# Performance work log

Hardware: AMD Instinct MI355X
Metric: run time of the kernel (lower is better)

Reference implementation:

```python
import jax, jax.numpy as jnp
import numpy as np
from jax import lax

B, T, D, H, C, FF, NH = 256, 48, 89, 128, 64, 64, 8
HD = C // NH


def _pos_encoding(n, c):
    pos = jnp.arange(n, dtype=jnp.float32)[:, None]
    div = jnp.exp(jnp.arange(0, c, 2, dtype=jnp.float32) * (-np.log(10000.0) / c))
    pe = jnp.zeros((n, c), dtype=jnp.float32)
    pe = pe.at[:, 0::2].set(jnp.sin(pos * div))
    pe = pe.at[:, 1::2].set(jnp.cos(pos * div))
    return pe


def _ln(x, g, b):
    m = x.mean(-1, keepdims=True)
    v = ((x - m) ** 2).mean(-1, keepdims=True)
    return (x - m) / jnp.sqrt(v + 1e-5) * g + b


def setup_inputs():
    key = jax.random.key(0)
    ks = iter(jax.random.split(key, 64))
    def n(shape, s=0.05):
        return (jax.random.normal(next(ks), shape) * s).astype(jnp.float32)
    x = jax.random.normal(next(ks), (B, T, D), dtype=jnp.float32)
    mask = (jax.random.uniform(next(ks), (B, T, D)) < 0.8).astype(jnp.float32)
    deltas = (jax.random.uniform(next(ks), (B, T, D)) * 5.0).astype(jnp.float32)
    last_obs = jax.random.normal(next(ks), (B, T, D), dtype=jnp.float32)
    medians = (jax.random.uniform(next(ks), (D,)) * 2.0).astype(jnp.float32)
    return dict(
        x=x, mask=mask, deltas=deltas, last_obs=last_obs, medians=medians,
        W_dh=n((H, D)), b_dh=n((H,)), W_dx=n((D, D)), b_dx=n((D,)),
        W_hist=n((D, H)), b_hist=n((D,)), W_feat=n((D, D)), b_feat=n((D,)),
        W_wc=n((D, 2 * D)), b_wc=n((D,)), W_wo=n((D, D)), b_wo=n((D,)),
        W_cls=n((1, H)), b_cls=n((1,)),
        W_ih=n((3 * H, 2 * D)), W_hh=n((3 * H, H)), b_ih=n((3 * H,)), b_hh=n((3 * H,)),
        W_inp=n((C, D)), b_inp=n((C,)), W_op1=n((H, C)), b_op1=n((H,)),
        W_op2=n((2 * T,)), b_op2=n((1,)),
        attn_in_w=n((3 * C, C)), attn_in_b=n((3 * C,)),
        attn_out_w=n((C, C)), attn_out_b=n((C,)),
        ln1_g=jnp.ones((C,)), ln1_b=jnp.zeros((C,)),
        ln2_g=jnp.ones((C,)), ln2_b=jnp.zeros((C,)),
        ff1_w=n((FF, C)), ff1_b=n((FF,)), ff2_w=n((C, FF)), ff2_b=n((C,)))


def _forward(x, mask, deltas, last_obs, medians,
             W_dh, b_dh, W_dx, b_dx, W_hist, b_hist, W_feat, b_feat,
             W_wc, b_wc, W_wo, b_wo, W_cls, b_cls,
             W_ih, W_hh, b_ih, b_hh, W_inp, b_inp, W_op1, b_op1, W_op2, b_op2,
             attn_in_w, attn_in_b, attn_out_w, attn_out_b,
             ln1_g, ln1_b, ln2_g, ln2_b, ff1_w, ff1_b, ff2_w, ff2_b):
    # Decay_obs: weight = 0.5*(1 - tanh(sign(dd)*|linear(dd)|))
    dd = deltas - medians[None, None, :]
    wd = dd @ W_wo.T + b_wo
    decay_factor = 0.5 * (1.0 - jnp.tanh(jnp.sign(dd) * jnp.abs(wd)))

    # time encoder: 1x1 conv projection + positional encoding
    pe = _pos_encoding(T, C)[None]                      # [1,T,C]
    d_lo = last_obs @ W_inp.T + b_inp + pe              # [B,T,C]
    d_df = decay_factor @ W_inp.T + b_inp + pe          # [B,T,C]
    data = jnp.concatenate([d_lo, d_df], axis=1)        # [B,2T,C]

    # torch TransformerEncoderLayer (post-norm, gelu, dropout off).
    # NOTE: layer is NOT batch_first, so attention runs over axis 0 (B);
    # axis 1 (2T) behaves as the batch — faithful to the source.
    qkv = data @ attn_in_w.T + attn_in_b                # [B,2T,3C]
    q, k, v = jnp.split(qkv, 3, axis=-1)
    q = q.reshape(B, 2 * T, NH, HD)
    k = k.reshape(B, 2 * T, NH, HD)
    v = v.reshape(B, 2 * T, NH, HD)
    scores = jnp.einsum('snhd,tnhd->nhst', q, k) / np.sqrt(HD)
    probs = jax.nn.softmax(scores, axis=-1)
    o = jnp.einsum('nhst,tnhd->snhd', probs, v).reshape(B, 2 * T, C)
    o = o @ attn_out_w.T + attn_out_b
    x1 = _ln(data + o, ln1_g, ln1_b)
    ff = jax.nn.gelu(x1 @ ff1_w.T + ff1_b, approximate=False) @ ff2_w.T + ff2_b
    data = _ln(x1 + ff, ln2_g, ln2_b)                   # [B,2T,C]

    data = data @ W_op1.T + b_op1                       # [B,2T,H]
    h0 = jnp.einsum('bnh,n->bh', data, W_op2) + b_op2[0]  # Conv1d(2T->1,k=1)

    diag_w = jnp.diagonal(W_dx)                         # temp_decay_x diag mask
    offdiag = 1.0 - jnp.eye(D, dtype=x.dtype)

    def step(carry, inp):
        h, loss = carry
        x_t, m_t, d_t = inp
        gamma_h = jnp.exp(-jax.nn.relu(d_t @ W_dh.T + b_dh))
        h = h * gamma_h
        x_h = h @ W_hist.T + b_hist
        x_r = m_t * x_t + (1.0 - m_t) * x_h
        xu = x_r @ (W_feat * offdiag).T + b_feat
        gamma_x = jnp.exp(-jax.nn.relu(d_t * diag_w + b_dx))
        beta = jnp.concatenate([gamma_x, m_t], axis=-1) @ W_wc.T + b_wc
        x_comb = beta * xu + (1.0 - beta) * x_h
        loss = loss + jnp.sum(jnp.abs(x_t - x_comb) * m_t) / (jnp.sum(m_t) + 1e-5)
        x_imp_t = m_t * x_t + (1.0 - m_t) * x_comb
        gi = jnp.concatenate([x_imp_t, m_t], axis=-1) @ W_ih.T + b_ih
        gh = h @ W_hh.T + b_hh
        ir, iz, ig = jnp.split(gi, 3, axis=-1)
        hr, hz, hg = jnp.split(gh, 3, axis=-1)
        r = jax.nn.sigmoid(ir + hr)
        z = jax.nn.sigmoid(iz + hz)
        g = jnp.tanh(ig + r * hg)
        h = (1.0 - z) * g + z * h
        return (h, loss), (x_imp_t, h)

    xs = (x.transpose(1, 0, 2), mask.transpose(1, 0, 2), deltas.transpose(1, 0, 2))
    (h, x_loss), (x_imp_T, hid_T) = lax.scan(step, (h0, jnp.zeros((), x.dtype)), xs)
    x_imp = x_imp_T.transpose(1, 0, 2)                  # [B,T,D]
    hiddens = hid_T.transpose(1, 0, 2)                  # [B,T,H]

    y_out = h @ W_cls.T + b_cls
    y_score = jax.nn.sigmoid(y_out)
    return x_imp, x_loss, hiddens, y_out, y_score


def reference(x, mask, deltas, last_obs, medians,
              W_dh, b_dh, W_dx, b_dx, W_hist, b_hist, W_feat, b_feat,
              W_wc, b_wc, W_wo, b_wo, W_cls, b_cls,
              W_ih, W_hh, b_ih, b_hh, W_inp, b_inp, W_op1, b_op1, W_op2, b_op2,
              attn_in_w, attn_in_b, attn_out_w, attn_out_b,
              ln1_g, ln1_b, ln2_g, ln2_b, ff1_w, ff1_b, ff2_w, ff2_b):
    return _forward(x, mask, deltas, last_obs, medians,
                    W_dh, b_dh, W_dx, b_dx, W_hist, b_hist, W_feat, b_feat,
                    W_wc, b_wc, W_wo, b_wo, W_cls, b_cls,
                    W_ih, W_hh, b_ih, b_hh, W_inp, b_inp, W_op1, b_op1, W_op2, b_op2,
                    attn_in_w, attn_in_b, attn_out_w, attn_out_b,
                    ln1_g, ln1_b, ln2_g, ln2_b, ff1_w, ff1_b, ff2_w, ff2_b)
```

## Files before the change

kernel.cpp:

```cpp
#include <hip/hip_runtime.h>
#include <math.h>

#define B_  256
#define T_  48
#define D_  89
#define H_  128
#define C_  64
#define NH_ 8
#define HD_ 8
#define N2T 96

#define XIMP_OFF 0
#define LOSS_OFF 1093632
#define HID_OFF  1093633
#define Y_OFF    2666497
#define YS_OFF   2666753

typedef unsigned int uint_t;
typedef _Float16 h2_t __attribute__((ext_vector_type(2)));

__device__ __forceinline__ float wave_sum64(float v) {
    v += __shfl_xor(v, 32);
    v += __shfl_xor(v, 16);
    v += __shfl_xor(v, 8);
    v += __shfl_xor(v, 4);
    v += __shfl_xor(v, 2);
    v += __shfl_xor(v, 1);
    return v;
}

__device__ __forceinline__ uint_t packh2(float lo, float hi) {
    union { h2_t h; uint_t u; } c;
    c.h.x = (_Float16)lo;
    c.h.y = (_Float16)hi;
    return c.u;
}
__device__ __forceinline__ h2_t as_h2(uint_t u) {
    union { uint_t u; h2_t h; } c;
    c.u = u;
    return c.h;
}
__device__ __forceinline__ float dot2h(uint_t w, uint_t a, float acc) {
#if __has_builtin(__builtin_amdgcn_fdot2)
    return __builtin_amdgcn_fdot2(as_h2(w), as_h2(a), acc, false);
#else
    h2_t hw = as_h2(w), ha = as_h2(a);
    return fmaf((float)hw.y, (float)ha.y, fmaf((float)hw.x, (float)ha.x, acc));
#endif
}
__device__ __forceinline__ float sigm(float v) { return 1.f / (1.f + __expf(-v)); }

#define DOT96H(W, A, acc) do { \
    _Pragma("unroll") \
    for (int it_ = 0; it_ < 3; ++it_) { \
        int idx_ = jj + 8 * it_; \
        uint2 w_ = ((const uint2*)(W))[idx_]; \
        uint2 a_ = ((const uint2*)(A))[idx_]; \
        acc = dot2h(w_.x, a_.x, acc); \
        acc = dot2h(w_.y, a_.y, acc); \
    } } while (0)

#define DOT128H(W, A, acc) do { \
    _Pragma("unroll") \
    for (int it_ = 0; it_ < 4; ++it_) { \
        int idx_ = jj + 8 * it_; \
        uint2 w_ = ((const uint2*)(W))[idx_]; \
        uint2 a_ = ((const uint2*)(A))[idx_]; \
        acc = dot2h(w_.x, a_.x, acc); \
        acc = dot2h(w_.y, a_.y, acc); \
    } } while (0)

__device__ __forceinline__ void tr_f32(const float* __restrict__ s, float* __restrict__ d,
                                       int li, int R, int C) {
    int r = li / C, c = li - r * C;
    d[c * R + r] = s[li];
}

__global__ void k_wprep(const float* W_wo, const float* W_inp, const float* ain_w,
                        const float* aout_w, const float* ff1_w, const float* ff2_w,
                        const float* W_op1,
                        float* W_woT, float* W_inpT, float* ain_T,
                        float* aout_T, float* ff1_T, float* ff2_T, float* op1_T,
                        const float* __restrict__ W_dh, const float* __restrict__ W_hist,
                        const float* __restrict__ W_ih, const float* __restrict__ W_hh,
                        uint_t* __restrict__ wdh_h, uint_t* __restrict__ whist_h,
                        uint_t* __restrict__ wihx_h, uint_t* __restrict__ wihm_h,
                        uint_t* __restrict__ whh_h) {
    int i = blockIdx.x * 256 + threadIdx.x;
    if (i < 7921)         tr_f32(W_wo,   W_woT,  i,          89, 89);
    else if (i < 13617)   tr_f32(W_inp,  W_inpT, i - 7921,   64, 89);
    else if (i < 25905)   tr_f32(ain_w,  ain_T,  i - 13617, 192, 64);
    else if (i < 30001)   tr_f32(aout_w, aout_T, i - 25905,  64, 64);
    else if (i < 34097)   tr_f32(ff1_w,  ff1_T,  i - 30001,  64, 64);
    else if (i < 38193)   tr_f32(ff2_w,  ff2_T,  i - 34097,  64, 64);
    else if (i < 46385)   tr_f32(W_op1,  op1_T,  i - 38193, 128, 64);
    else {
        int p = i - 46385;
        if (p < 6144) {
            int r = p / 48, c = p - r * 48;
            const float* src = W_dh + r * 89;
            float lo = (c < 45) ? src[2 * c] : 0.f;
            float hi = (c < 44) ? src[2 * c + 1] : 0.f;
            wdh_h[p] = packh2(lo, hi);
        } else if (p < 11840) {
            int j = p - 6144;
            int r = j / 64, c = j - r * 64;
            const float* src = W_hist + r * 128;
            whist_h[j] = packh2(src[2 * c], src[2 * c + 1]);
        } else if (p < 30272) {
            int j = p - 11840;
            int r = j / 48, c = j - r * 48;
            const float* src = W_ih + (size_t)r * 178;
            float lo = (c < 45) ? src[2 * c] : 0.f;
            float hi = (c < 44) ? src[2 * c + 1] : 0.f;
            wihx_h[j] = packh2(lo, hi);
        } else if (p < 48704) {
            int j = p - 30272;
            int r = j / 48, c = j - r * 48;
            const float* src = W_ih + (size_t)r * 178 + 89;
            float lo = (c < 45) ? src[2 * c] : 0.f;
            float hi = (c < 44) ? src[2 * c + 1] : 0.f;
            wihm_h[j] = packh2(lo, hi);
        } else if (p < 73280) {
            int j = p - 48704;
            int r = j / 64, c = j - r * 64;
            const float* src = W_hh + (size_t)r * 128;
            whh_h[j] = packh2(src[2 * c], src[2 * c + 1]);
        }
    }
}

__global__ void k_phaseA(const float* __restrict__ last_obs,
                         const float* __restrict__ deltas,
                         const float* __restrict__ medians,
                         const float* __restrict__ W_woT, const float* __restrict__ b_wo,
                         const float* __restrict__ W_inpT, const float* __restrict__ b_inp,
                         const float* __restrict__ ain_T, const float* __restrict__ ain_b,
                         float* __restrict__ data,
                         float* __restrict__ qb, float* __restrict__ kb, float* __restrict__ vb) {
    int bt = blockIdx.x;
    int b = bt / T_;
    int t = bt - b * T_;
    __shared__ float dd[D_], lo[D_], dec[D_];
    __shared__ float rows[2][C_];
    int tid = threadIdx.x;
    int base = (b * T_ + t) * D_;
    if (tid < D_) {
        float dv = deltas[base + tid] - medians[tid];
        dd[tid] = dv;
        lo[tid] = last_obs[base + tid];
    }
    __syncthreads();
    if (tid < D_) {
        float a0 = b_wo[tid], a1 = 0.f;
        for (int j = 0; j < 88; j += 2) {
            a0 = fmaf(dd[j],     W_woT[j * D_ + tid],       a0);
            a1 = fmaf(dd[j + 1], W_woT[(j + 1) * D_ + tid], a1);
        }
        float acc = fmaf(dd[88], W_woT[88 * D_ + tid], a0) + a1;
        float dv = dd[tid];
        float s = (dv > 0.f) ? 1.f : ((dv < 0.f) ? -1.f : 0.f);
        dec[tid] = 0.5f * (1.f - tanhf(s * fabsf(acc)));
    }
    __syncthreads();
    int c = tid & 63;
    int half = tid >> 6;
    {
        const float* src = half ? dec : lo;
        float a0 = b_inp[c], a1 = 0.f;
        for (int j = 0; j < 88; j += 2) {
            a0 = fmaf(src[j],     W_inpT[j * C_ + c],       a0);
            a1 = fmaf(src[j + 1], W_inpT[(j + 1) * C_ + c], a1);
        }
        float acc = fmaf(src[88], W_inpT[88 * C_ + c], a0) + a1;
        int i = c >> 1;
        float div = __expf((float)i * -0.28782313662425574f);
        float ang = (float)t * div;
        float pe = (c & 1) ? cosf(ang) : sinf(ang);
        float val = acc + pe;
        rows[half][c] = val;
        data[((b * N2T) + half * T_ + t) * C_ + c] = val;
    }
    __syncthreads();
    #pragma unroll
    for (int it = 0; it < 3; ++it) {
        int idx = it * 128 + tid;
        int h2 = idx / 192;
        int col = idx - h2 * 192;
        const float* row = rows[h2];
        float a0 = ain_b[col], a1 = 0.f;
        #pragma unroll
        for (int j = 0; j < 64; j += 2) {
            a0 = fmaf(row[j],     ain_T[j * 192 + col],       a0);
            a1 = fmaf(row[j + 1], ain_T[(j + 1) * 192 + col], a1);
        }
        float acc = a0 + a1;
        int n = h2 * T_ + t;
        int part = col >> 6;
        int cc = col & 63;
        int hh = cc >> 3, d = cc & 7;
        float* dst = (part == 0) ? qb : ((part == 1) ? kb : vb);
        dst[(((n * NH_ + hh) * B_ + b) * HD_) + d] = acc;
    }
}

__global__ void k_attn(const float* __restrict__ qb, const float* __restrict__ kb,
                       const float* __restrict__ vb, float* __restrict__ attnO) {
    int n = blockIdx.x >> 3;
    int h = blockIdx.x & 7;
    __shared__ float k_lds[B_][HD_ + 1];
    __shared__ float v_lds[B_][HD_ + 1];
    int s = threadIdx.x;
    const float scale = 0.35355339059327373f;
    size_t base = ((size_t)blockIdx.x * B_ + s) * HD_;
    float q[HD_];
    #pragma unroll
    for (int d = 0; d < HD_; ++d) q[d] = qb[base + d] * scale;
    #pragma unroll
    for (int d = 0; d < HD_; ++d) { k_lds[s][d] = kb[base + d]; v_lds[s][d] = vb[base + d]; }
    __syncthreads();
    float m = -1e30f;
    #pragma unroll 4
    for (int t = 0; t < B_; ++t) {
        float sc = 0.f;
        #pragma unroll
        for (int d = 0; d < HD_; ++d) sc = fmaf(q[d], k_lds[t][d], sc);
        m = fmaxf(m, sc);
    }
    float l = 0.f;
    float acc[HD_] = {0.f, 0.f, 0.f, 0.f, 0.f, 0.f, 0.f, 0.f};
    #pragma unroll 2
    for (int t = 0; t < B_; ++t) {
        float sc = 0.f;
        #pragma unroll
        for (int d = 0; d < HD_; ++d) sc = fmaf(q[d], k_lds[t][d], sc);
        float p = __expf(sc - m);
        l += p;
        #pragma unroll
        for (int d = 0; d < HD_; ++d) acc[d] = fmaf(p, v_lds[t][d], acc[d]);
    }
    float inv = 1.f / l;
    float* op = attnO + ((size_t)s * N2T + n) * C_ + h * HD_;
    #pragma unroll
    for (int d = 0; d < HD_; ++d) op[d] = acc[d] * inv;
}

__global__ void k_transform(const float* __restrict__ data,
                            const float* __restrict__ attnO,
                            const float* __restrict__ aout_T, const float* __restrict__ aout_b,
                            const float* __restrict__ ln1_g, const float* __restrict__ ln1_b,
                            const float* __restrict__ ff1_T, const float* __restrict__ ff1_b,
                            const float* __restrict__ ff2_T, const float* __restrict__ ff2_b,
                            const float* __restrict__ ln2_g, const float* __restrict__ ln2_b,
                            const float* __restrict__ op1_T, const float* __restrict__ b_op1,
                            float* __restrict__ val) {
    int bn = blockIdx.x;
    __shared__ float orow[C_], x1s[C_], hbuf[C_], x2s[C_];
    int c = threadIdx.x;
    float d0 = data[bn * C_ + c];
    orow[c] = attnO[bn * C_ + c];
    __syncthreads();
    float a0 = aout_b[c], a1 = 0.f;
    #pragma unroll
    for (int j = 0; j < C_; j += 2) {
        a0 = fmaf(orow[j],     aout_T[j * C_ + c],       a0);
        a1 = fmaf(orow[j + 1], aout_T[(j + 1) * C_ + c], a1);
    }
    float r = d0 + a0 + a1;
    float mean = wave_sum64(r) * (1.f / 64.f);
    float df = r - mean;
    float var = wave_sum64(df * df) * (1.f / 64.f);
    float x1 = df * rsqrtf(var + 1e-5f) * ln1_g[c] + ln1_b[c];
    x1s[c] = x1;
    __syncthreads();
    a0 = ff1_b[c]; a1 = 0.f;
    #pragma unroll
    for (int j = 0; j < C_; j += 2) {
        a0 = fmaf(x1s[j],     ff1_T[j * C_ + c],       a0);
        a1 = fmaf(x1s[j + 1], ff1_T[(j + 1) * C_ + c], a1);
    }
    float accf = a0 + a1;
    float ge = 0.5f * accf * (1.f + erff(accf * 0.7071067811865475f));
    hbuf[c] = ge;
    __syncthreads();
    a0 = ff2_b[c]; a1 = 0.f;
    #pragma unroll
    for (int j = 0; j < C_; j += 2) {
        a0 = fmaf(hbuf[j],     ff2_T[j * C_ + c],       a0);
        a1 = fmaf(hbuf[j + 1], ff2_T[(j + 1) * C_ + c], a1);
    }
    float r2 = x1 + a0 + a1;
    float mean2 = wave_sum64(r2) * (1.f / 64.f);
    float df2 = r2 - mean2;
    float var2 = wave_sum64(df2 * df2) * (1.f / 64.f);
    float x2 = df2 * rsqrtf(var2 + 1e-5f) * ln2_g[c] + ln2_b[c];
    x2s[c] = x2;
    __syncthreads();
    #pragma unroll
    for (int rep = 0; rep < 2; ++rep) {
        int k = c + rep * 64;
        float b0 = b_op1[k], b1 = 0.f;
        #pragma unroll
        for (int j = 0; j < C_; j += 2) {
            b0 = fmaf(x2s[j],     op1_T[j * H_ + k],       b0);
            b1 = fmaf(x2s[j + 1], op1_T[(j + 1) * H_ + k], b1);
        }
        val[(size_t)bn * H_ + k] = b0 + b1;
    }
}

__global__ void k_reduce_h0(const float* __restrict__ val,
                            const float* __restrict__ W_op2, const float* __restrict__ b_op2,
                            float* __restrict__ h0) {
    int b = blockIdx.x;
    int h = threadIdx.x;
    float a0 = b_op2[0], a1 = 0.f;
    for (int n = 0; n < N2T; n += 2) {
        a0 = fmaf(val[((size_t)b * N2T + n) * H_ + h],       W_op2[n],     a0);
        a1 = fmaf(val[((size_t)b * N2T + n + 1) * H_ + h],   W_op2[n + 1], a1);
    }
    h0[b * H_ + h] = a0 + a1;
}

__global__ void k_den(const float* __restrict__ mask, float* __restrict__ den) {
    int t = blockIdx.x;
    int tid = threadIdx.x;
    float s = 0.f;
    const int total = B_ * D_;
    for (int i = tid; i < total; i += 256) {
        int b = i / D_;
        int d = i - b * D_;
        s += mask[(b * T_ + t) * D_ + d];
    }
    s = wave_sum64(s);
    __shared__ float red[4];
    if ((tid & 63) == 0) red[tid >> 6] = s;
    __syncthreads();
    if (tid == 0) den[t] = red[0] + red[1] + red[2] + red[3];
}

__global__ __launch_bounds__(1024)
void k_scan(const float* __restrict__ x, const float* __restrict__ mask,
            const float* __restrict__ deltas,
            const uint_t* __restrict__ wdh_h, const float* __restrict__ b_dh,
            const float* __restrict__ W_dx, const float* __restrict__ b_dx,
            const uint_t* __restrict__ whist_h, const float* __restrict__ b_hist,
            const float* __restrict__ W_feat, const float* __restrict__ b_feat,
            const float* __restrict__ W_wc, const float* __restrict__ b_wc,
            const uint_t* __restrict__ wihx_h, const uint_t* __restrict__ wihm_h,
            const uint_t* __restrict__ whh_h,
            const float* __restrict__ b_ih, const float* __restrict__ b_hh,
            const float* __restrict__ W_cls, const float* __restrict__ b_cls,
            const float* __restrict__ h0,
            float* __restrict__ out, float* __restrict__ num_part) {
    int b = blockIdx.x;
    int tid = threadIdx.x;
    int wave = tid >> 6;
    int lane = tid & 63;
    int oo = lane >> 3;
    int jj = lane & 7;

    __shared__ __align__(16) float h_s[H_];
    __shared__ __align__(16) uint_t h_h[64];
    __shared__ __align__(16) float xt_s[96], m_s[96], xh_s[96], beta_s[96], diff_s[96];
    __shared__ __align__(16) uint_t dt_h[48], gx_h[48], m_h[48], xr_h[48], ximp_h[48];
    __shared__ __align__(16) float gis[384], ghs[384];
    __shared__ __align__(16) uint_t wwcg_l[89 * 48];
    __shared__ __align__(16) uint_t wwcm_l[89 * 48];
    __shared__ __align__(16) uint_t wfeat_l[89 * 48];

    float dxw = 0.f, dxb = 0.f;
    if (tid >= 384 && tid < 473) {
        int o = tid - 384;
        dxw = W_dx[o * 90];
        dxb = b_dx[o];
    }

    for (int i = tid; i < 89 * 48; i += 1024) {
        int r = i / 48, c = i - r * 48;
        const float* wr = W_wc + (size_t)r * 178;
        float lo = (c < 45) ? wr[2 * c] : 0.f;
        float hi = (c < 44) ? wr[2 * c + 1] : 0.f;
        wwcg_l[i] = packh2(lo, hi);
        const float* wm = wr + 89;
        float lo2 = (c < 45) ? wm[2 * c] : 0.f;
        float hi2 = (c < 44) ? wm[2 * c + 1] : 0.f;
        wwcm_l[i] = packh2(lo2, hi2);
        const float* wf = W_feat + r * 89;
        float lo3 = (c < 45 && 2 * c != r) ? wf[2 * c] : 0.f;
        float hi3 = (c < 44 && 2 * c + 1 != r) ? wf[2 * c + 1] : 0.f;
        wfeat_l[i] = packh2(lo3, hi3);
    }
    if (tid < 128) {
        float hv = h0[b * H_ + tid];
        h_s[tid] = hv;
        float nx = __shfl_down(hv, 1);
        if ((tid & 1) == 0) h_h[tid >> 1] = packh2(hv, nx);
    }
    if (tid == 500) {
        #pragma unroll
        for (int k = 45; k < 48; ++k) {
            dt_h[k] = 0u; gx_h[k] = 0u; m_h[k] = 0u; xr_h[k] = 0u; ximp_h[k] = 0u;
        }
    }
    {
        int nb = b * T_ * D_;
        if (tid >= 128 && tid < 217) xt_s[tid - 128] = x[nb + tid - 128];
        else if (tid >= 256 && tid < 345) {
            int o = tid - 256;
            float mv = mask[nb + o];
            m_s[o] = mv;
            float nx = __shfl_down(mv, 1);
            if (o + 1 >= 89) nx = 0.f;
            if ((o & 1) == 0) m_h[o >> 1] = packh2(mv, nx);
        } else if (tid >= 384 && tid < 473) {
            int o = tid - 384;
            float dv = deltas[nb + o];
            float gxv = __expf(-fmaxf(dv * dxw + dxb, 0.f));
            float nd = __shfl_down(dv, 1);
            float ng = __shfl_down(gxv, 1);
            if (o + 1 >= 89) { nd = 0.f; ng = 0.f; }
            if ((o & 1) == 0) { dt_h[o >> 1] = packh2(dv, nd); gx_h[o >> 1] = packh2(gxv, ng); }
        }
    }
    __syncthreads();

    for (int t = 0; t < T_; ++t) {
        for (int c = wave; c < 76; c += 16) {
            if (c < 16) {
                int o = c * 8 + oo;
                float acc = 0.f;
                DOT96H(wdh_h + o * 48, dt_h, acc);
                acc += __shfl_xor(acc, 1); acc += __shfl_xor(acc, 2); acc += __shfl_xor(acc, 4);
                if (jj == 0) {
                    float hv = h_s[o] * __expf(-fmaxf(acc + b_dh[o], 0.f));
                    h_s[o] = hv;
                    float nx = __shfl_down(hv, 8);
                    if ((oo & 1) == 0) h_h[o >> 1] = packh2(hv, nx);
                }
            } else if (c < 28) {
                int o = (c - 16) * 8 + oo;
                int ro = (o < 89) ? o : 88;
                float acc = 0.f;
                DOT96H(wwcg_l + ro * 48, gx_h, acc);
                DOT96H(wwcm_l + ro * 48, m_h, acc);
                acc += __shfl_xor(acc, 1); acc += __shfl_xor(acc, 2); acc += __shfl_xor(acc, 4);
                if (jj == 0 && o < 89) beta_s[o] = acc + b_wc[o];
            } else {
                int o = (c - 28) * 8 + oo;
                float acc = 0.f;
                DOT96H(wihm_h + o * 48, m_h, acc);
                acc += __shfl_xor(acc, 1); acc += __shfl_xor(acc, 2); acc += __shfl_xor(acc, 4);
                if (jj == 0) gis[o] = acc + b_ih[o];
            }
        }
        __syncthreads();
        for (int c = wave; c < 60; c += 16) {
            if (c < 12) {
                int o = c * 8 + oo;
                int ro = (o < 89) ? o : 88;
                float acc = 0.f;
                DOT128H(whist_h + ro * 64, h_h, acc);
                acc += __shfl_xor(acc, 1); acc += __shfl_xor(acc, 2); acc += __shfl_xor(acc, 4);
                if (jj == 0) {
                    float xh = acc + b_hist[ro];
                    float m = m_s[ro];
                    float xrv = m * xt_s[ro] + (1.f - m) * xh;
                    float nx = __shfl_down(xrv, 8);
                    if (o + 1 >= 89) nx = 0.f;
                    if (o < 89) xh_s[o] = xh;
                    if ((oo & 1) == 0 && o < 89) xr_h[o >> 1] = packh2(xrv, nx);
                }
            } else {
                int o = (c - 12) * 8 + oo;
                float acc = 0.f;
                DOT128H(whh_h + o * 64, h_h, acc);
                acc += __shfl_xor(acc, 1); acc += __shfl_xor(acc, 2); acc += __shfl_xor(acc, 4);
                if (jj == 0) ghs[o] = acc + b_hh[o];
            }
        }
        __syncthreads();
        for (int c = wave; c < 12; c += 16) {
            int o = c * 8 + oo;
            int ro = (o < 89) ? o : 88;
            float xu = 0.f;
            DOT96H(wfeat_l + ro * 48, xr_h, xu);
            xu += __shfl_xor(xu, 1); xu += __shfl_xor(xu, 2); xu += __shfl_xor(xu, 4);
            if (jj == 0) {
                float xuf = xu + b_feat[ro];
                float btf = beta_s[ro];
                float xc = btf * xuf + (1.f - btf) * xh_s[ro];
                float m = m_s[ro];
                float xtv = xt_s[ro];
                float xi = m * xtv + (1.f - m) * xc;
                float nx = __shfl_down(xi, 8);
                if (o + 1 >= 89) nx = 0.f;
                if (o < 89) {
                    out[XIMP_OFF + (b * T_ + t) * D_ + o] = xi;
                    diff_s[o] = fabsf(xtv - xc) * m;
                }
                if ((oo & 1) == 0 && o < 89) ximp_h[o >> 1] = packh2(xi, nx);
            }
        }
        __syncthreads();
        for (int c = wave; c < 48; c += 16) {
            int o = c * 8 + oo;
            float acc = 0.f;
            DOT96H(wihx_h + o * 48, ximp_h, acc);
            acc += __shfl_xor(acc, 1); acc += __shfl_xor(acc, 2); acc += __shfl_xor(acc, 4);
            if (jj == 0) gis[o] += acc;
        }
        __syncthreads();
        if (tid < 128) {
            float r = sigm(gis[tid] + ghs[tid]);
            float z = sigm(gis[128 + tid] + ghs[128 + tid]);
            float g = tanhf(gis[256 + tid] + r * ghs[256 + tid]);
            float hn = (1.f - z) * g + z * h_s[tid];
            h_s[tid] = hn;
            out[HID_OFF + (size_t)(b * T_ + t) * H_ + tid] = hn;
            float nx = __shfl_down(hn, 1);
            if ((tid & 1) == 0) h_h[tid >> 1] = packh2(hn, nx);
        } else if (tid >= 960) {
            int l = tid - 960;
            float s = diff_s[l] + ((l < 25) ? diff_s[64 + l] : 0.f);
            s = wave_sum64(s);
            if (l == 0) num_part[t * B_ + b] = s;
        } else if (t + 1 < T_) {
            int nb = (b * T_ + t + 1) * D_;
            if (tid < 217) xt_s[tid - 128] = x[nb + tid - 128];
            else if (tid >= 256 && tid < 345) {
                int o = tid - 256;
                float mv = mask[nb + o];
                m_s[o] = mv;
                float nx = __shfl_down(mv, 1);
                if (o + 1 >= 89) nx = 0.f;
                if ((o & 1) == 0) m_h[o >> 1] = packh2(mv, nx);
            } else if (tid >= 384 && tid < 473) {
                int o = tid - 384;
                float dv = deltas[nb + o];
                float gxv = __expf(-fmaxf(dv * dxw + dxb, 0.f));
                float nd = __shfl_down(dv, 1);
                float ng = __shfl_down(gxv, 1);
                if (o + 1 >= 89) { nd = 0.f; ng = 0.f; }
                if ((o & 1) == 0) { dt_h[o >> 1] = packh2(dv, nd); gx_h[o >> 1] = packh2(gxv, ng); }
            }
        }
        __syncthreads();
    }
    if (tid < 64) {
        float p = h_s[tid] * W_cls[tid] + h_s[tid + 64] * W_cls[tid + 64];
        p = wave_sum64(p);
        if (tid == 0) {
            float y = p + b_cls[0];
            out[Y_OFF + b] = y;
            out[YS_OFF + b] = 1.f / (1.f + __expf(-y));
        }
    }
}

__global__ void k_loss(const float* __restrict__ num_part, const float* __restrict__ den,
                       float* __restrict__ out) {
    int tid = threadIdx.x;
    float v = 0.f;
    if (tid < T_) {
        float s = 0.f;
        const float* np_ = num_part + tid * B_;
        for (int b = 0; b < B_; ++b) s += np_[b];
        v = s / (den[tid] + 1e-5f);
    }
    v = wave_sum64(v);
    if (tid == 0) out[LOSS_OFF] = v;
}

extern "C" void kernel_launch(void* const* d_in, const int* in_sizes, int n_in,
                              void* d_out, int out_size, void* d_ws, size_t ws_size,
                              hipStream_t stream) {
    const float* x        = (const float*)d_in[0];
    const float* mask     = (const float*)d_in[1];
    const float* deltas   = (const float*)d_in[2];
    const float* last_obs = (const float*)d_in[3];
    const float* medians  = (const float*)d_in[4];
    const float* W_dh  = (const float*)d_in[5];
    const float* b_dh  = (const float*)d_in[6];
    const float* W_dx  = (const float*)d_in[7];
    const float* b_dx  = (const float*)d_in[8];
    const float* W_hist= (const float*)d_in[9];
    const float* b_hist= (const float*)d_in[10];
    const float* W_feat= (const float*)d_in[11];
    const float* b_feat= (const float*)d_in[12];
    const float* W_wc  = (const float*)d_in[13];
    const float* b_wc  = (const float*)d_in[14];
    const float* W_wo  = (const float*)d_in[15];
    const float* b_wo  = (const float*)d_in[16];
    const float* W_cls = (const float*)d_in[17];
    const float* b_cls = (const float*)d_in[18];
    const float* W_ih  = (const float*)d_in[19];
    const float* W_hh  = (const float*)d_in[20];
    const float* b_ih  = (const float*)d_in[21];
    const float* b_hh  = (const float*)d_in[22];
    const float* W_inp = (const float*)d_in[23];
    const float* b_inp = (const float*)d_in[24];
    const float* W_op1 = (const float*)d_in[25];
    const float* b_op1 = (const float*)d_in[26];
    const float* W_op2 = (const float*)d_in[27];
    const float* b_op2 = (const float*)d_in[28];
    const float* attn_in_w  = (const float*)d_in[29];
    const float* attn_in_b  = (const float*)d_in[30];
    const float* attn_out_w = (const float*)d_in[31];
    const float* attn_out_b = (const float*)d_in[32];
    const float* ln1_g = (const float*)d_in[33];
    const float* ln1_b = (const float*)d_in[34];
    const float* ln2_g = (const float*)d_in[35];
    const float* ln2_b = (const float*)d_in[36];
    const float* ff1_w = (const float*)d_in[37];
    const float* ff1_b = (const float*)d_in[38];
    const float* ff2_w = (const float*)d_in[39];
    const float* ff2_b = (const float*)d_in[40];

    float* out = (float*)d_out;
    float* ws = (float*)d_ws;

    float* data  = ws;
    float* qb    = data  + (size_t)B_ * N2T * C_;
    float* kb    = qb    + (size_t)N2T * NH_ * B_ * HD_;
    float* vb    = kb    + (size_t)N2T * NH_ * B_ * HD_;
    float* attnO = vb    + (size_t)N2T * NH_ * B_ * HD_;
    float* val   = attnO + (size_t)B_ * N2T * C_;
    float* h0    = val   + (size_t)B_ * N2T * H_;
    float* den   = h0    + (size_t)B_ * H_;
    float* nump  = den   + 64;
    float* W_woT = nump  + T_ * B_;
    float* W_inpT= W_woT + 7921;
    float* ain_T = W_inpT + 5696;
    float* aout_T= ain_T + 12288;
    float* ff1_T = aout_T + 4096;
    float* ff2_T = ff1_T + 4096;
    float* op1_T = ff2_T + 4096;
    uint_t* wdh_h   = (uint_t*)(op1_T + 8192);
    uint_t* whist_h = wdh_h + 6144;
    uint_t* wihx_h  = whist_h + 5696;
    uint_t* wihm_h  = wihx_h + 18432;
    uint_t* whh_h   = wihm_h + 18432;

    k_wprep<<<468, 256, 0, stream>>>(W_wo, W_inp, attn_in_w, attn_out_w, ff1_w, ff2_w, W_op1,
                                     W_woT, W_inpT, ain_T, aout_T, ff1_T, ff2_T, op1_T,
                                     W_dh, W_hist, W_ih, W_hh,
                                     wdh_h, whist_h, wihx_h, wihm_h, whh_h);
    k_phaseA<<<B_ * T_, 128, 0, stream>>>(last_obs, deltas, medians, W_woT, b_wo, W_inpT, b_inp,
                                          ain_T, attn_in_b, data, qb, kb, vb);
    k_attn<<<N2T * NH_, 256, 0, stream>>>(qb, kb, vb, attnO);
    k_transform<<<B_ * N2T, 64, 0, stream>>>(data, attnO, aout_T, attn_out_b,
                                             ln1_g, ln1_b, ff1_T, ff1_b, ff2_T, ff2_b,
                                             ln2_g, ln2_b, op1_T, b_op1, val);
    k_reduce_h0<<<B_, H_, 0, stream>>>(val, W_op2, b_op2, h0);
    k_den<<<T_, 256, 0, stream>>>(mask, den);
    k_scan<<<B_, 1024, 0, stream>>>(x, mask, deltas,
                                    wdh_h, b_dh, W_dx, b_dx, whist_h, b_hist, W_feat, b_feat,
                                    W_wc, b_wc, wihx_h, wihm_h, whh_h, b_ih, b_hh, W_cls, b_cls,
                                    h0, out, nump);
    k_loss<<<1, 64, 0, stream>>>(nump, den, out);
}
```

Measured before the change: 588.3 us.

## Fold hidden decay into GRU update and merge two phases to drop a barrier

The temporal-decay product (W_dh·delta, then exp) for step t+1 is now computed by the GRU-update threads at the end of step t. It uses a padded LDS copy of W_dh (row stride 49 to avoid bank conflicts), and the deltas for t+1 are loaded earlier, during the feature-regression phase. This removes a separate phase, so the beta/gate-input and history/hidden-gate matvecs run in one loop with one fewer __syncthreads per timestep. In exchange, the 128 GRU threads each do a serial 45-term dot product, and the extra LDS allocation may lower occupancy.

Result: no change. 587.6 us (median of 2 runs) (-0.1%).

```diff
diff --git a/kernel.cpp b/kernel.cpp
--- a/kernel.cpp
+++ b/kernel.cpp
@@ -368,10 +368,11 @@
     __shared__ __align__(16) uint_t wwcg_l[89 * 48];
     __shared__ __align__(16) uint_t wwcm_l[89 * 48];
     __shared__ __align__(16) uint_t wfeat_l[89 * 48];
+    __shared__ __align__(16) uint_t wdh_l[128 * 49];
 
     float dxw = 0.f, dxb = 0.f;
-    if (tid >= 384 && tid < 473) {
-        int o = tid - 384;
+    if (tid >= 768 && tid < 857) {
+        int o = tid - 768;
         dxw = W_dx[o * 90];
         dxb = b_dx[o];
     }
@@ -391,11 +392,9 @@
         float hi3 = (c < 44 && 2 * c + 1 != r) ? wf[2 * c + 1] : 0.f;
         wfeat_l[i] = packh2(lo3, hi3);
     }
-    if (tid < 128) {
-        float hv = h0[b * H_ + tid];
-        h_s[tid] = hv;
-        float nx = __shfl_down(hv, 1);
-        if ((tid & 1) == 0) h_h[tid >> 1] = packh2(hv, nx);
+    for (int i = tid; i < 128 * 45; i += 1024) {
+        int r = i / 45, c = i - r * 45;
+        wdh_l[r * 49 + c] = wdh_h[r * 48 + c];
     }
     if (tid == 500) {
         #pragma unroll
@@ -403,6 +402,8 @@
             dt_h[k] = 0u; gx_h[k] = 0u; m_h[k] = 0u; xr_h[k] = 0u; ximp_h[k] = 0u;
         }
     }
+    float h0v = 0.f;
+    if (tid < 128) h0v = h0[b * H_ + tid];
     {
         int nb = b * T_ * D_;
         if (tid >= 128 && tid < 217) xt_s[tid - 128] = x[nb + tid - 128];
@@ -413,8 +414,8 @@
             float nx = __shfl_down(mv, 1);
             if (o + 1 >= 89) nx = 0.f;
             if ((o & 1) == 0) m_h[o >> 1] = packh2(mv, nx);
-        } else if (tid >= 384 && tid < 473) {
-            int o = tid - 384;
+        } else if (tid >= 768 && tid < 857) {
+            int o = tid - 768;
             float dv = deltas[nb + o];
             float gxv = __expf(-fmaxf(dv * dxw + dxb, 0.f));
             float nd = __shfl_down(dv, 1);
@@ -424,40 +425,36 @@
         }
     }
     __syncthreads();
+    if (tid < 128) {
+        const uint_t* wr = wdh_l + tid * 49;
+        float acc = 0.f;
+        #pragma unroll
+        for (int j = 0; j < 45; ++j) acc = dot2h(wr[j], dt_h[j], acc);
+        float hd = h0v * __expf(-fmaxf(acc + b_dh[tid], 0.f));
+        h_s[tid] = hd;
+        float nx = __shfl_down(hd, 1);
+        if ((tid & 1) == 0) h_h[tid >> 1] = packh2(hd, nx);
+    }
+    __syncthreads();
 
     for (int t = 0; t < T_; ++t) {
-        for (int c = wave; c < 76; c += 16) {
-            if (c < 16) {
+        for (int c = wave; c < 120; c += 16) {
+            if (c < 12) {
                 int o = c * 8 + oo;
-                float acc = 0.f;
-                DOT96H(wdh_h + o * 48, dt_h, acc);
-                acc += __shfl_xor(acc, 1); acc += __shfl_xor(acc, 2); acc += __shfl_xor(acc, 4);
-                if (jj == 0) {
-                    float hv = h_s[o] * __expf(-fmaxf(acc + b_dh[o], 0.f));
-                    h_s[o] = hv;
-                    float nx = __shfl_down(hv, 8);
-                    if ((oo & 1) == 0) h_h[o >> 1] = packh2(hv, nx);
-                }
-            } else if (c < 28) {
-                int o = (c - 16) * 8 + oo;
                 int ro = (o < 89) ? o : 88;
                 float acc = 0.f;
                 DOT96H(wwcg_l + ro * 48, gx_h, acc);
                 DOT96H(wwcm_l + ro * 48, m_h, acc);
                 acc += __shfl_xor(acc, 1); acc += __shfl_xor(acc, 2); acc += __shfl_xor(acc, 4);
                 if (jj == 0 && o < 89) beta_s[o] = acc + b_wc[o];
-            } else {
-                int o = (c - 28) * 8 + oo;
+            } else if (c < 60) {
+                int o = (c - 12) * 8 + oo;
                 float acc = 0.f;
                 DOT96H(wihm_h + o * 48, m_h, acc);
                 acc += __shfl_xor(acc, 1); acc += __shfl_xor(acc, 2); acc += __shfl_xor(acc, 4);
                 if (jj == 0) gis[o] = acc + b_ih[o];
-            }
-        }
-        __syncthreads();
-        for (int c = wave; c < 60; c += 16) {
-            if (c < 12) {
-                int o = c * 8 + oo;
+            } else if (c < 72) {
+                int o = (c - 60) * 8 + oo;
                 int ro = (o < 89) ? o : 88;
                 float acc = 0.f;
                 DOT128H(whist_h + ro * 64, h_h, acc);
@@ -472,7 +469,7 @@
                     if ((oo & 1) == 0 && o < 89) xr_h[o >> 1] = packh2(xrv, nx);
                 }
             } else {
-                int o = (c - 12) * 8 + oo;
+                int o = (c - 72) * 8 + oo;
                 float acc = 0.f;
                 DOT128H(whh_h + o * 64, h_h, acc);
                 acc += __shfl_xor(acc, 1); acc += __shfl_xor(acc, 2); acc += __shfl_xor(acc, 4);
@@ -480,7 +477,8 @@
             }
         }
         __syncthreads();
-        for (int c = wave; c < 12; c += 16) {
+        if (wave < 12) {
+            int c = wave;
             int o = c * 8 + oo;
             int ro = (o < 89) ? o : 88;
             float xu = 0.f;
@@ -501,6 +499,14 @@
                 }
                 if ((oo & 1) == 0 && o < 89) ximp_h[o >> 1] = packh2(xi, nx);
             }
+        } else if (tid >= 768 && tid < 857 && t + 1 < T_) {
+            int o = tid - 768;
+            float dv = deltas[(b * T_ + t + 1) * D_ + o];
+            float gxv = __expf(-fmaxf(dv * dxw + dxb, 0.f));
+            float nd = __shfl_down(dv, 1);
+            float ng = __shfl_down(gxv, 1);
+            if (o + 1 >= 89) { nd = 0.f; ng = 0.f; }
+            if ((o & 1) == 0) { dt_h[o >> 1] = packh2(dv, nd); gx_h[o >> 1] = packh2(gxv, ng); }
         }
         __syncthreads();
         for (int c = wave; c < 48; c += 16) {
@@ -516,10 +522,18 @@
             float z = sigm(gis[128 + tid] + ghs[128 + tid]);
             float g = tanhf(gis[256 + tid] + r * ghs[256 + tid]);
             float hn = (1.f - z) * g + z * h_s[tid];
-            h_s[tid] = hn;
             out[HID_OFF + (size_t)(b * T_ + t) * H_ + tid] = hn;
-            float nx = __shfl_down(hn, 1);
-            if ((tid & 1) == 0) h_h[tid >> 1] = packh2(hn, nx);
+            float hd = hn;
+            if (t + 1 < T_) {
+                const uint_t* wr = wdh_l + tid * 49;
+                float acc = 0.f;
+                #pragma unroll
+                for (int j = 0; j < 45; ++j) acc = dot2h(wr[j], dt_h[j], acc);
+                hd = hn * __expf(-fmaxf(acc + b_dh[tid], 0.f));
+            }
+            h_s[tid] = hd;
+            float nx = __shfl_down(hd, 1);
+            if ((tid & 1) == 0) h_h[tid >> 1] = packh2(hd, nx);
         } else if (tid >= 960) {
             int l = tid - 960;
             float s = diff_s[l] + ((l < 25) ? diff_s[64 + l] : 0.f);
@@ -535,14 +549,6 @@
                 float nx = __shfl_down(mv, 1);
                 if (o + 1 >= 89) nx = 0.f;
                 if ((o & 1) == 0) m_h[o >> 1] = packh2(mv, nx);
-            } else if (tid >= 384 && tid < 473) {
-                int o = tid - 384;
-                float dv = deltas[nb + o];
-                float gxv = __expf(-fmaxf(dv * dxw + dxb, 0.f));
-                float nd = __shfl_down(dv, 1);
-                float ng = __shfl_down(gxv, 1);
-                if (o + 1 >= 89) { nd = 0.f; ng = 0.f; }
-                if ((o & 1) == 0) { dt_h[o >> 1] = packh2(dv, nd); gx_h[o >> 1] = packh2(gxv, ng); }
             }
         }
         __syncthreads();
```
